# Kernel optimization log

Hardware: AMD Instinct MI355X
Metric: run time of the kernel (lower is better)

## Reference

```python
import jax, jax.numpy as jnp
import numpy as np

B, T, S, A = 8, 256, 16, 1
H, NH, L, NI, TIME, TMAX = 1024, 16, 6, 4096, 8, 512
NEG = -10000.0


def _ln(x, g, b, eps=1e-5):
    m = jnp.mean(x, -1, keepdims=True)
    v = jnp.mean((x - m) ** 2, -1, keepdims=True)
    return (x - m) * jax.lax.rsqrt(v + eps) * g + b


def setup_inputs() -> dict:
    key = jax.random.key(0)
    ks = iter(jax.random.split(key, 64))
    w = lambda *s: 0.02 * jax.random.normal(next(ks), s, jnp.float32)
    inp = {
        'states': jax.random.normal(next(ks), (B, T, S), jnp.float32),
        'actions': jax.random.normal(next(ks), (B, T, A), jnp.float32),
        'rtgs': jax.random.normal(next(ks), (B, T, 1), jnp.float32),
        'attention_mask': jnp.ones((B, T, 1), jnp.float32),
        'state_mean': jnp.zeros((S,), jnp.float32),
        'state_std': jnp.ones((S,), jnp.float32),
        'W_es': w(S, H), 'b_es': jnp.zeros((H,)),
        'W_ea': w(A, H), 'b_ea': jnp.zeros((H,)),
        'W_er': w(1, H), 'b_er': jnp.zeros((H,)),
        'E_t': w(TMAX, TIME),
        'W_ts': w(H + TIME, H), 'b_ts': jnp.zeros((H,)),
        'W_ta': w(H + TIME, H), 'b_ta': jnp.zeros((H,)),
        'W_tr': w(H + TIME, H), 'b_tr': jnp.zeros((H,)),
        'eln_g': jnp.ones((H,)), 'eln_b': jnp.zeros((H,)),
        'ln1_g': jnp.ones((L, H)), 'ln1_b': jnp.zeros((L, H)),
        'ln2_g': jnp.ones((L, H)), 'ln2_b': jnp.zeros((L, H)),
        'Wq': w(L, H, H), 'bq': jnp.zeros((L, H)),
        'Wk': w(L, H, H), 'bk': jnp.zeros((L, H)),
        'Wv': w(L, H, H), 'bv': jnp.zeros((L, H)),
        'Wo': w(L, H, H), 'bo': jnp.zeros((L, H)),
        'W1': w(L, H, NI), 'b1': jnp.zeros((L, NI)),
        'W2': w(L, NI, H), 'b2': jnp.zeros((L, H)),
        'W_pa': w(H, A), 'b_pa': jnp.zeros((A,)),
        'timesteps': jax.random.randint(next(ks), (B, T), 0, TMAX),
    }
    return inp


def _forward(states, actions, rtgs, attention_mask, state_mean, state_std,
             W_es, b_es, W_ea, b_ea, W_er, b_er, E_t,
             W_ts, b_ts, W_ta, b_ta, W_tr, b_tr, eln_g, eln_b,
             ln1_g, ln1_b, ln2_g, ln2_b, Wq, bq, Wk, bk, Wv, bv, Wo, bo,
             W1, b1, W2, b2, W_pa, b_pa, timesteps):
    T3 = 3 * T
    dh = H // NH
    s = (states - state_mean) / (state_std + 1e-9)
    te = E_t[timesteps]                                   # [B,T,8]
    se = jnp.concatenate([s @ W_es + b_es, te], -1) @ W_ts + b_ts
    ae = jnp.concatenate([actions @ W_ea + b_ea, te], -1) @ W_ta + b_ta
    re = jnp.concatenate([rtgs @ W_er + b_er, te], -1) @ W_tr + b_tr
    # interleave (rtg, state, action) per timestep -> [B, 3T, H]
    x = jnp.stack([re, se, ae], axis=2).reshape(B, T3, H)
    x = _ln(x, eln_g, eln_b)

    timestep_mask = jnp.max(attention_mask, axis=-1)      # [B,T]
    pad = (1.0 - jnp.repeat(timestep_mask, 3, axis=1)) * NEG  # [B,3T]
    pad = pad[:, None, None, :]
    causal = jnp.tril(jnp.ones((T3, T3), bool))

    def block(x, p):
        (l1g, l1b, wq, bqv, wk, bkv, wv, bvv, wo, bov,
         l2g, l2b, w1, b1v, w2, b2v) = p
        h = _ln(x, l1g, l1b)
        def heads(w, b):
            return (h @ w + b).reshape(B, T3, NH, dh).transpose(0, 2, 1, 3)
        q, k, v = heads(wq, bqv), heads(wk, bkv), heads(wv, bvv)
        att = jnp.einsum('bhqd,bhkd->bhqk', q, k) / jnp.sqrt(jnp.float32(dh))
        att = jnp.where(causal, att, jnp.asarray(NEG, att.dtype)) + pad
        att = jax.nn.softmax(att, axis=-1)
        y = jnp.einsum('bhqk,bhkd->bhqd', att, v)
        y = y.transpose(0, 2, 1, 3).reshape(B, T3, H) @ wo + bov
        x = x + y
        m = _ln(x, l2g, l2b)
        x = x + jax.nn.gelu(m @ w1 + b1v, approximate=False) @ w2 + b2v
        return x, None

    stacked = (ln1_g, ln1_b, Wq, bq, Wk, bk, Wv, bv, Wo, bo,
               ln2_g, ln2_b, W1, b1, W2, b2)
    x, _ = jax.lax.scan(block, x, stacked)

    x = x.reshape(B, T, 3, H)
    action_preds = x[:, :, 1] @ W_pa + b_pa               # state-token positions
    return action_preds


def reference(states, actions, rtgs, attention_mask, state_mean, state_std,
              W_es, b_es, W_ea, b_ea, W_er, b_er, E_t,
              W_ts, b_ts, W_ta, b_ta, W_tr, b_tr, eln_g, eln_b,
              ln1_g, ln1_b, ln2_g, ln2_b, Wq, bq, Wk, bk, Wv, bv, Wo, bo,
              W1, b1, W2, b2, W_pa, b_pa, timesteps):
    return _forward(states, actions, rtgs, attention_mask, state_mean, state_std,
                    W_es, b_es, W_ea, b_ea, W_er, b_er, E_t,
                    W_ts, b_ts, W_ta, b_ta, W_tr, b_tr, eln_g, eln_b,
                    ln1_g, ln1_b, ln2_g, ln2_b, Wq, bq, Wk, bk, Wv, bv, Wo, bo,
                    W1, b1, W2, b2, W_pa, b_pa, timesteps)
```

## Files before the change

kernel.cpp:

```cpp
#include <hip/hip_runtime.h>
#include <math.h>

#define B_    8
#define T_    256
#define S_    16
#define H_    1024
#define NH_   16
#define L_    6
#define NI_   4096
#define TIME_ 8
#define T3_   768
#define DH_   64
#define BT_   2048
#define ROWS_ 6144
#define KE_   1032
#define KEP_  1056
#define NEGV  (-10000.0f)

typedef unsigned short u16;
typedef short bf16x8 __attribute__((ext_vector_type(8)));
typedef float f32x4 __attribute__((ext_vector_type(4)));

__device__ __forceinline__ float bf2f(u16 u) {
    union { unsigned int i; float f; } x; x.i = ((unsigned int)u) << 16; return x.f;
}
__device__ __forceinline__ u16 f2bf(float f) {
    union { float f; unsigned int i; } x; x.f = f;
    unsigned int r = x.i + 0x7FFFu + ((x.i >> 16) & 1u);
    return (u16)(r >> 16);
}
__device__ __forceinline__ float gelu_fast(float x) {
    float y = 0.7978845608028654f * (x + 0.044715f * x * x * x);
    float e = __expf(2.0f * y);
    float t = 1.0f - 2.0f / (e + 1.0f);
    return 0.5f * x * (1.0f + t);
}

__device__ __forceinline__ void gll16(const u16* g, u16* l) {
    __builtin_amdgcn_global_load_lds(
        (const __attribute__((address_space(1))) unsigned int*)g,
        (__attribute__((address_space(3))) unsigned int*)l,
        16, 0, 0);
}

template <int EPI, int BM>
__device__ __forceinline__ void mgemm_core(
    const u16* __restrict__ A, const u16* __restrict__ Bt,
    const float* __restrict__ bias, float* __restrict__ outf,
    u16* __restrict__ outb, const float* __restrict__ res,
    int N, int K)
{
    constexpr int MT = (BM == 128) ? 4 : 2;
    __shared__ u16 Als[2][BM * 32];
    __shared__ u16 Bls[2][128 * 32];
    const int tid = threadIdx.x;

    const int nbx = N >> 7;
    const int bid = blockIdx.x;
    const int G = nbx << 3;
    const int grp = bid / G;
    const int g = bid - grp * G;
    const int bm = (grp * 8 + (g & 7)) * BM;
    const int bn = (g >> 3) * 128;

    const int lane = tid & 63;
    const int w = tid >> 6;
    const int wr = (BM == 128) ? (w >> 1) : (w & 1);
    const int wc = (BM == 128) ? (w & 1) : (w >> 1);
    const int lrow = lane & 15;
    const int lk = lane >> 4;

    f32x4 acc[MT][4] = {};

    auto stage = [&](int buf, int kk) {
        if (BM == 128) {
            #pragma unroll
            for (int s = 0; s < 2; ++s) {
                const int gb = w * 64 + s * 256;
                const int j = gb >> 7, m0 = gb & 127;
                gll16(A + (size_t)(bm + m0 + lane) * K + kk + j * 8, Als[buf] + gb * 8);
            }
        } else {
            gll16(A + (size_t)(bm + lane) * K + kk + w * 8, Als[buf] + w * 64 * 8);
        }
        #pragma unroll
        for (int s = 0; s < 2; ++s) {
            const int gb = w * 64 + s * 256;
            const int j = gb >> 7, m0 = gb & 127;
            gll16(Bt + (size_t)(bn + m0 + lane) * K + kk + j * 8, Bls[buf] + gb * 8);
        }
    };

    const int niter = K >> 5;
    stage(0, 0);
    for (int i = 0; i < niter; ++i) {
        __syncthreads();
        if (i + 1 < niter) stage((i + 1) & 1, (i + 1) * 32);
        const bf16x8* Af = (const bf16x8*)Als[i & 1];
        const bf16x8* Bf = (const bf16x8*)Bls[i & 1];
        bf16x8 af[MT], bfr[4];
        #pragma unroll
        for (int tm = 0; tm < MT; ++tm)
            af[tm] = Af[lk * BM + wr * (MT * 16) + tm * 16 + lrow];
        #pragma unroll
        for (int tn = 0; tn < 4; ++tn)
            bfr[tn] = Bf[lk * 128 + wc * 64 + tn * 16 + lrow];
        #pragma unroll
        for (int tm = 0; tm < MT; ++tm)
            #pragma unroll
            for (int tn = 0; tn < 4; ++tn)
                acc[tm][tn] = __builtin_amdgcn_mfma_f32_16x16x32_bf16(
                    af[tm], bfr[tn], acc[tm][tn], 0, 0, 0);
    }

    int cg[4]; float bv[4];
    #pragma unroll
    for (int tn = 0; tn < 4; ++tn) {
        cg[tn] = bn + wc * 64 + tn * 16 + lrow;
        bv[tn] = bias[cg[tn]];
    }
    #pragma unroll
    for (int tm = 0; tm < MT; ++tm) {
        const int rbase = bm + wr * (MT * 16) + tm * 16 + lk * 4;
        #pragma unroll
        for (int r = 0; r < 4; ++r) {
            const size_t rowoff = (size_t)(rbase + r) * N;
            #pragma unroll
            for (int tn = 0; tn < 4; ++tn) {
                float v = acc[tm][tn][r] + bv[tn];
                const size_t idx = rowoff + cg[tn];
                if (EPI == 0) outf[idx] = v;
                else if (EPI == 1) outf[idx] = v + res[idx];
                else if (EPI == 2) outb[idx] = f2bf(v);
                else { outb[idx] = f2bf(gelu_fast(v)); }
            }
        }
    }
}

template <int EPI, int BM>
__global__ __launch_bounds__(256) void mgemm(
    const u16* __restrict__ A, const u16* __restrict__ Bt,
    const float* __restrict__ bias, float* __restrict__ outf,
    u16* __restrict__ outb, const float* __restrict__ res,
    int N, int K)
{
    mgemm_core<EPI, BM>(A, Bt, bias, outf, outb, res, N, K);
}

__global__ __launch_bounds__(256) void mgemm_embed(
    const u16* __restrict__ U, const u16* __restrict__ Wt,
    const float* __restrict__ b0, const float* __restrict__ b1,
    const float* __restrict__ b2, float* __restrict__ out)
{
    const int z = blockIdx.z;
    const float* bias = (z == 0) ? b0 : (z == 1) ? b1 : b2;
    mgemm_core<0, 64>(U + (size_t)z * BT_ * KEP_, Wt + (size_t)z * H_ * KEP_,
                      bias, out + (size_t)z * BT_ * H_, nullptr, nullptr,
                      H_, KEP_);
}

__device__ __forceinline__ void convT_core(
    const float* __restrict__ W, u16* __restrict__ Wt, int K, int N, int Kpad)
{
    __shared__ float tile[32][65];
    const int k0 = blockIdx.y * 32, n0 = blockIdx.x * 64;
    const int tid = threadIdx.x;
    #pragma unroll
    for (int p = 0; p < 2; ++p) {
        const int kr = (tid >> 4) + p * 16;
        const int nc = (tid & 15) * 4;
        const int k = k0 + kr;
        float4 v = make_float4(0.f, 0.f, 0.f, 0.f);
        if (k < K) v = *(const float4*)(W + (size_t)k * N + n0 + nc);
        tile[kr][nc + 0] = v.x; tile[kr][nc + 1] = v.y;
        tile[kr][nc + 2] = v.z; tile[kr][nc + 3] = v.w;
    }
    __syncthreads();
    #pragma unroll
    for (int p = 0; p < 2; ++p) {
        const int idx = tid + p * 256;
        const int n = idx >> 3, kq = (idx & 7) * 4;
        ushort4 o;
        o.x = f2bf(tile[kq + 0][n]); o.y = f2bf(tile[kq + 1][n]);
        o.z = f2bf(tile[kq + 2][n]); o.w = f2bf(tile[kq + 3][n]);
        *(ushort4*)(Wt + (size_t)(n0 + n) * Kpad + k0 + kq) = o;
    }
}

__global__ __launch_bounds__(256) void convTv(
    const float* __restrict__ W, u16* __restrict__ Wt, int K, int N, int Kpad)
{
    convT_core(W, Wt, K, N, Kpad);
}

__global__ __launch_bounds__(256) void convT_embed(
    const float* __restrict__ W0, const float* __restrict__ W1,
    const float* __restrict__ W2, u16* __restrict__ Wt)
{
    const int z = blockIdx.z;
    const float* W = (z == 0) ? W0 : (z == 1) ? W1 : W2;
    convT_core(W, Wt + (size_t)z * H_ * KEP_, KE_, H_, KEP_);
}

__global__ __launch_bounds__(256) void convT4v(
    const float* __restrict__ Wq, const float* __restrict__ Wk,
    const float* __restrict__ Wv, const float* __restrict__ Wo,
    const float* __restrict__ bq, const float* __restrict__ bk,
    const float* __restrict__ bv,
    u16* __restrict__ WQKVt, u16* __restrict__ Wot, float* __restrict__ bqkv)
{
    const int z = blockIdx.z;
    const float* W = (z == 0) ? Wq : (z == 1) ? Wk : (z == 2) ? Wv : Wo;
    u16* Wt = (z == 3) ? Wot : WQKVt + (size_t)z * H_ * H_;
    convT_core(W, Wt, H_, H_, H_);
    if (blockIdx.x == 0 && blockIdx.y == 0 && z < 3) {
        const float* bsrc = (z == 0) ? bq : (z == 1) ? bk : bv;
        #pragma unroll
        for (int u = 0; u < 4; ++u) {
            int i = threadIdx.x + u * 256;
            bqkv[z * H_ + i] = bsrc[i];
        }
    }
}

__global__ __launch_bounds__(256) void embed_pre_kernel(
    const float* __restrict__ states, const float* __restrict__ actions,
    const float* __restrict__ rtgs, const float* __restrict__ mean,
    const float* __restrict__ stdv, const float* __restrict__ W_es,
    const float* __restrict__ b_es, const float* __restrict__ W_ea,
    const float* __restrict__ b_ea, const float* __restrict__ W_er,
    const float* __restrict__ b_er, const float* __restrict__ E_t,
    const int* __restrict__ timesteps,
    u16* __restrict__ Us, u16* __restrict__ Ua, u16* __restrict__ Ur)
{
    const int bt  = blockIdx.x;
    const int tid = threadIdx.x;
    __shared__ float sn[S_];
    __shared__ float tev[TIME_];
    if (tid < S_) sn[tid] = (states[bt * S_ + tid] - mean[tid]) / (stdv[tid] + 1e-9f);
    if (tid < TIME_) {
        int ts = timesteps[bt];
        tev[tid] = E_t[ts * TIME_ + tid];
    }
    __syncthreads();
    const float av = actions[bt];
    const float rv = rtgs[bt];
    const size_t rowo = (size_t)bt * KEP_;
    #pragma unroll
    for (int u = 0; u < 4; ++u) {
        int n = tid + u * 256;
        float accs = b_es[n];
        #pragma unroll
        for (int i = 0; i < S_; ++i) accs += sn[i] * W_es[i * H_ + n];
        Us[rowo + n] = f2bf(accs);
        Ua[rowo + n] = f2bf(av * W_ea[n] + b_ea[n]);
        Ur[rowo + n] = f2bf(rv * W_er[n] + b_er[n]);
    }
    if (tid < TIME_) {
        u16 tv = f2bf(tev[tid]);
        Us[rowo + H_ + tid] = tv;
        Ua[rowo + H_ + tid] = tv;
        Ur[rowo + H_ + tid] = tv;
    }
    if (tid < KEP_ - KE_) {
        Us[rowo + KE_ + tid] = 0;
        Ua[rowo + KE_ + tid] = 0;
        Ur[rowo + KE_ + tid] = 0;
    }
}

template <bool BF16OUT>
__device__ __forceinline__ void ln_body(const float* __restrict__ src,
                                        const float* __restrict__ g,
                                        const float* __restrict__ b,
                                        void* __restrict__ dst,
                                        float* red, int tid)
{
    float v[4];
    #pragma unroll
    for (int u = 0; u < 4; ++u) v[u] = src[tid + u * 256];
    float s = v[0] + v[1] + v[2] + v[3];
    red[tid] = s; __syncthreads();
    for (int off = 128; off > 0; off >>= 1) {
        if (tid < off) red[tid] += red[tid + off];
        __syncthreads();
    }
    const float mean = red[0] * (1.0f / H_);
    __syncthreads();
    float ss = 0.0f;
    #pragma unroll
    for (int u = 0; u < 4; ++u) { float d = v[u] - mean; ss += d * d; }
    red[tid] = ss; __syncthreads();
    for (int off = 128; off > 0; off >>= 1) {
        if (tid < off) red[tid] += red[tid + off];
        __syncthreads();
    }
    const float var = red[0] * (1.0f / H_);
    const float rs = rsqrtf(var + 1e-5f);
    #pragma unroll
    for (int u = 0; u < 4; ++u) {
        int col = tid + u * 256;
        float y = (v[u] - mean) * rs * g[col] + b[col];
        if (BF16OUT) ((u16*)dst)[col] = f2bf(y);
        else ((float*)dst)[col] = y;
    }
}

__global__ __launch_bounds__(256) void ln_bf16_kernel(
    const float* __restrict__ X, const float* __restrict__ g,
    const float* __restrict__ b, u16* __restrict__ Y)
{
    __shared__ float red[256];
    const size_t row = blockIdx.x;
    ln_body<true>(X + row * H_, g, b, Y + row * H_, red, threadIdx.x);
}

__global__ __launch_bounds__(256) void interleave_eln_kernel(
    const float* __restrict__ RE, const float* __restrict__ SE,
    const float* __restrict__ AE, const float* __restrict__ g,
    const float* __restrict__ b, float* __restrict__ X)
{
    __shared__ float red[256];
    const int row = blockIdx.x;
    const int bi = row / T3_;
    const int rem = row % T3_;
    const int t = rem / 3, slot = rem % 3;
    const float* src = (slot == 0 ? RE : (slot == 1 ? SE : AE)) + (size_t)(bi * T_ + t) * H_;
    ln_body<false>(src, g, b, X + (size_t)row * H_, red, threadIdx.x);
}

__global__ __launch_bounds__(256) void attn_kernel(
    const u16* __restrict__ QKV, const float* __restrict__ amask,
    u16* __restrict__ Y)
{
    const int qt = blockIdx.x;
    const int h  = blockIdx.y;
    const int b  = blockIdx.z;
    const int tid = threadIdx.x;
    const int lane = tid & 63, w = tid >> 6;
    const int l15 = lane & 15, quad = lane >> 4;

    __shared__ u16 Kls[64][72];
    __shared__ u16 Vt[64][72];
    __shared__ u16 Pls[4][16][72];
    __shared__ float padv[64];

    const u16* Qbase = QKV + (size_t)b * T3_ * 3072 + h * 64;
    const u16* Kbase = Qbase + 1024;
    const u16* Vbase = Qbase + 2048;

    bf16x8 qf[2];
    {
        const u16* qp = Qbase + (size_t)(qt * 64 + w * 16 + l15) * 3072 + quad * 8;
        qf[0] = *(const bf16x8*)qp;
        qf[1] = *(const bf16x8*)(qp + 32);
    }

    float m_i[4], l_i[4];
    f32x4 o[4] = {};
    #pragma unroll
    for (int r = 0; r < 4; ++r) { m_i[r] = -3.0e30f; l_i[r] = 0.0f; }

    const int qr0 = qt * 64 + w * 16 + quad * 4;

    for (int kt = 0; kt <= qt; ++kt) {
        #pragma unroll
        for (int s = 0; s < 2; ++s) {
            const int c = tid + s * 256;
            const int tok = c >> 3, cb = c & 7;
            const size_t go = (size_t)(kt * 64 + tok) * 3072 + cb * 8;
            *(uint4*)&Kls[tok][cb * 8] = *(const uint4*)(Kbase + go);
            uint4 vv = *(const uint4*)(Vbase + go);
            const u16* vs = (const u16*)&vv;
            #pragma unroll
            for (int j = 0; j < 8; ++j) Vt[cb * 8 + j][tok] = vs[j];
        }
        if (tid < 64)
            padv[tid] = (1.0f - amask[b * T_ + (kt * 64 + tid) / 3]) * NEGV;
        __syncthreads();

        f32x4 sacc[4];
        #pragma unroll
        for (int nt = 0; nt < 4; ++nt) {
            bf16x8 kf0 = *(const bf16x8*)&Kls[nt * 16 + l15][quad * 8];
            bf16x8 kf1 = *(const bf16x8*)&Kls[nt * 16 + l15][32 + quad * 8];
            f32x4 z = {};
            z = __builtin_amdgcn_mfma_f32_16x16x32_bf16(qf[0], kf0, z, 0, 0, 0);
            sacc[nt] = __builtin_amdgcn_mfma_f32_16x16x32_bf16(qf[1], kf1, z, 0, 0, 0);
        }

        float sv[4][4];
        float rmax[4] = {-3.0e30f, -3.0e30f, -3.0e30f, -3.0e30f};
        #pragma unroll
        for (int nt = 0; nt < 4; ++nt) {
            const int jc = kt * 64 + nt * 16 + l15;
            const float pv = padv[nt * 16 + l15];
            #pragma unroll
            for (int r = 0; r < 4; ++r) {
                float v = (jc <= qr0 + r) ? sacc[nt][r] * 0.125f : NEGV;
                v += pv;
                sv[nt][r] = v;
                rmax[r] = fmaxf(rmax[r], v);
            }
        }
        #pragma unroll
        for (int m = 1; m < 16; m <<= 1)
            #pragma unroll
            for (int r = 0; r < 4; ++r)
                rmax[r] = fmaxf(rmax[r], __shfl_xor(rmax[r], m, 64));
        float al[4], rsum[4];
        #pragma unroll
        for (int r = 0; r < 4; ++r) {
            const float mn = fmaxf(m_i[r], rmax[r]);
            al[r] = __expf(m_i[r] - mn);
            m_i[r] = mn;
            float sum = 0.0f;
            #pragma unroll
            for (int nt = 0; nt < 4; ++nt) {
                float p = __expf(sv[nt][r] - mn);
                sv[nt][r] = p; sum += p;
            }
            rsum[r] = sum;
        }
        #pragma unroll
        for (int m = 1; m < 16; m <<= 1)
            #pragma unroll
            for (int r = 0; r < 4; ++r)
                rsum[r] += __shfl_xor(rsum[r], m, 64);
        #pragma unroll
        for (int r = 0; r < 4; ++r)
            l_i[r] = l_i[r] * al[r] + rsum[r];

        #pragma unroll
        for (int nt = 0; nt < 4; ++nt)
            #pragma unroll
            for (int r = 0; r < 4; ++r)
                Pls[w][quad * 4 + r][nt * 16 + l15] = f2bf(sv[nt][r]);
        #pragma unroll
        for (int dt = 0; dt < 4; ++dt)
            #pragma unroll
            for (int r = 0; r < 4; ++r)
                o[dt][r] *= al[r];

        bf16x8 pf0 = *(const bf16x8*)&Pls[w][l15][quad * 8];
        bf16x8 pf1 = *(const bf16x8*)&Pls[w][l15][32 + quad * 8];
        #pragma unroll
        for (int dt = 0; dt < 4; ++dt) {
            bf16x8 vf0 = *(const bf16x8*)&Vt[dt * 16 + l15][quad * 8];
            bf16x8 vf1 = *(const bf16x8*)&Vt[dt * 16 + l15][32 + quad * 8];
            o[dt] = __builtin_amdgcn_mfma_f32_16x16x32_bf16(pf0, vf0, o[dt], 0, 0, 0);
            o[dt] = __builtin_amdgcn_mfma_f32_16x16x32_bf16(pf1, vf1, o[dt], 0, 0, 0);
        }
        __syncthreads();
    }

    #pragma unroll
    for (int r = 0; r < 4; ++r) {
        const float inv = 1.0f / l_i[r];
        const size_t row = (size_t)b * T3_ + qt * 64 + w * 16 + quad * 4 + r;
        #pragma unroll
        for (int dt = 0; dt < 4; ++dt)
            Y[row * H_ + h * 64 + dt * 16 + l15] = f2bf(o[dt][r] * inv);
    }
}

__global__ __launch_bounds__(256) void head_kernel(
    const float* __restrict__ X, const float* __restrict__ W_pa,
    const float* __restrict__ b_pa, float* __restrict__ out)
{
    __shared__ float red[256];
    const int row = blockIdx.x;
    const int b = row / T_, t = row % T_;
    const float* x = X + ((size_t)b * T3_ + 3 * t + 1) * H_;
    const int tid = threadIdx.x;
    float s = 0.0f;
    #pragma unroll
    for (int u = 0; u < 4; ++u) {
        int col = tid + u * 256;
        s += x[col] * W_pa[col];
    }
    red[tid] = s; __syncthreads();
    for (int off = 128; off > 0; off >>= 1) {
        if (tid < off) red[tid] += red[tid + off];
        __syncthreads();
    }
    if (tid == 0) out[row] = red[0] + b_pa[0];
}

extern "C" void kernel_launch(void* const* d_in, const int* in_sizes, int n_in,
                              void* d_out, int out_size, void* d_ws, size_t ws_size,
                              hipStream_t stream)
{
    const float* states  = (const float*)d_in[0];
    const float* actions = (const float*)d_in[1];
    const float* rtgs    = (const float*)d_in[2];
    const float* amask   = (const float*)d_in[3];
    const float* smean   = (const float*)d_in[4];
    const float* sstd    = (const float*)d_in[5];
    const float* W_es    = (const float*)d_in[6];
    const float* b_es    = (const float*)d_in[7];
    const float* W_ea    = (const float*)d_in[8];
    const float* b_ea    = (const float*)d_in[9];
    const float* W_er    = (const float*)d_in[10];
    const float* b_er    = (const float*)d_in[11];
    const float* E_t     = (const float*)d_in[12];
    const float* W_ts    = (const float*)d_in[13];
    const float* b_ts    = (const float*)d_in[14];
    const float* W_ta    = (const float*)d_in[15];
    const float* b_ta    = (const float*)d_in[16];
    const float* W_tr    = (const float*)d_in[17];
    const float* b_tr    = (const float*)d_in[18];
    const float* eln_g   = (const float*)d_in[19];
    const float* eln_b   = (const float*)d_in[20];
    const float* ln1_g   = (const float*)d_in[21];
    const float* ln1_b   = (const float*)d_in[22];
    const float* ln2_g   = (const float*)d_in[23];
    const float* ln2_b   = (const float*)d_in[24];
    const float* Wq      = (const float*)d_in[25];
    const float* bq      = (const float*)d_in[26];
    const float* Wk      = (const float*)d_in[27];
    const float* bk      = (const float*)d_in[28];
    const float* Wv      = (const float*)d_in[29];
    const float* bv      = (const float*)d_in[30];
    const float* Wo      = (const float*)d_in[31];
    const float* bo      = (const float*)d_in[32];
    const float* W1      = (const float*)d_in[33];
    const float* b1      = (const float*)d_in[34];
    const float* W2      = (const float*)d_in[35];
    const float* b2      = (const float*)d_in[36];
    const float* W_pa    = (const float*)d_in[37];
    const float* b_pa    = (const float*)d_in[38];
    const int*   tsteps  = (const int*)d_in[39];
    float* out = (float*)d_out;

    char* base = (char*)d_ws;
    float* X    = (float*)base;
    u16*   Hb   = (u16*)(base + 25165824);
    u16*   QKVb = (u16*)(base + 37748736);
    u16*   MIDb = (u16*)(base + 75497472);
    u16*   Wbuf = (u16*)(base + 125829120);

    float* bqkv = (float*)MIDb;
    u16* U_s = MIDb;
    u16* U_a = MIDb + (size_t)BT_ * KEP_;
    u16* U_r = MIDb + (size_t)2 * BT_ * KEP_;
    float* SE = (float*)QKVb;
    float* AE = SE + (size_t)BT_ * H_;
    float* RE = AE + (size_t)BT_ * H_;
    u16* Wemb = Wbuf;

    u16* WQKVt = Wbuf;
    u16* Wot   = Wbuf + (size_t)3072 * 1024;
    u16* W1t   = Wbuf + (size_t)4096 * 1024;
    u16* W2t   = Wbuf + (size_t)8192 * 1024;

    embed_pre_kernel<<<BT_, 256, 0, stream>>>(
        states, actions, rtgs, smean, sstd, W_es, b_es, W_ea, b_ea,
        W_er, b_er, E_t, tsteps, U_s, U_a, U_r);

    dim3 gCvE(H_ / 64, KEP_ / 32, 3);
    convT_embed<<<gCvE, 256, 0, stream>>>(W_ts, W_ta, W_tr, Wemb);

    dim3 gEmb((H_ / 128) * (BT_ / 64), 1, 3);
    mgemm_embed<<<gEmb, 256, 0, stream>>>(U_s, Wemb, b_ts, b_ta, b_tr, SE);

    interleave_eln_kernel<<<ROWS_, 256, 0, stream>>>(RE, SE, AE, eln_g, eln_b, X);

    dim3 gCv4(H_ / 64, H_ / 32, 4);
    dim3 gCvM1(NI_ / 64, H_ / 32);
    dim3 gCvM2(H_ / 64, NI_ / 32);
    const int gQKV = (3072 / 128) * (ROWS_ / 128);
    const int gO   = (H_ / 128) * (ROWS_ / 128);
    const int gM1  = (NI_ / 128) * (ROWS_ / 128);
    dim3 gAttn(T3_ / 64, NH_, B_);

    for (int l = 0; l < L_; ++l) {
        const size_t wOff = (size_t)l * H_ * H_;
        const size_t bOff = (size_t)l * H_;
        const size_t w1Off = (size_t)l * H_ * NI_;
        const size_t b1Off = (size_t)l * NI_;

        convT4v<<<gCv4, 256, 0, stream>>>(
            Wq + wOff, Wk + wOff, Wv + wOff, Wo + wOff,
            bq + bOff, bk + bOff, bv + bOff, WQKVt, Wot, bqkv);
        convTv<<<gCvM1, 256, 0, stream>>>(W1 + w1Off, W1t, H_, NI_, H_);
        convTv<<<gCvM2, 256, 0, stream>>>(W2 + w1Off, W2t, NI_, H_, NI_);

        ln_bf16_kernel<<<ROWS_, 256, 0, stream>>>(X, ln1_g + bOff, ln1_b + bOff, Hb);
        mgemm<2, 128><<<gQKV, 256, 0, stream>>>(Hb, WQKVt, bqkv, nullptr, QKVb, nullptr, 3072, H_);
        attn_kernel<<<gAttn, 256, 0, stream>>>(QKVb, amask, Hb);
        mgemm<1, 128><<<gO, 256, 0, stream>>>(Hb, Wot, bo + bOff, X, nullptr, X, H_, H_);
        ln_bf16_kernel<<<ROWS_, 256, 0, stream>>>(X, ln2_g + bOff, ln2_b + bOff, Hb);
        mgemm<3, 128><<<gM1, 256, 0, stream>>>(Hb, W1t, b1 + b1Off, nullptr, MIDb, nullptr, NI_, H_);
        mgemm<1, 128><<<gO, 256, 0, stream>>>(MIDb, W2t, b2 + bOff, X, nullptr, X, H_, NI_);
    }

    head_kernel<<<BT_, 256, 0, stream>>>(X, W_pa, b_pa, out);
}
```

Baseline: 3.206 ms.

## Split-K the Wo and W2 GEMMs with atomic accumulation into residual

Adds a split-K variant of the bf16 MFMA GEMM that divides K across two blockIdx.y slices and accumulates partial tiles directly into the fp32 residual stream with atomic adds. Only split 0 adds the bias. It is used for the output-projection and second MLP GEMMs, which have N=1024 and only 384 tiles, so the grid doubles to fill the CUs better. The cost is atomic traffic to X and non-deterministic summation order.

```diff
diff --git a/kernel.cpp b/kernel.cpp
--- a/kernel.cpp
+++ b/kernel.cpp
@@ -48,7 +48,7 @@
     const u16* __restrict__ A, const u16* __restrict__ Bt,
     const float* __restrict__ bias, float* __restrict__ outf,
     u16* __restrict__ outb, const float* __restrict__ res,
-    int N, int K)
+    int N, int K, int koff, int klen, bool addb)
 {
     constexpr int MT = (BM == 128) ? 4 : 2;
     __shared__ u16 Als[2][BM * 32];
@@ -91,11 +91,11 @@
         }
     };
 
-    const int niter = K >> 5;
-    stage(0, 0);
+    const int niter = klen >> 5;
+    stage(0, koff);
     for (int i = 0; i < niter; ++i) {
         __syncthreads();
-        if (i + 1 < niter) stage((i + 1) & 1, (i + 1) * 32);
+        if (i + 1 < niter) stage((i + 1) & 1, koff + (i + 1) * 32);
         const bf16x8* Af = (const bf16x8*)Als[i & 1];
         const bf16x8* Bf = (const bf16x8*)Bls[i & 1];
         bf16x8 af[MT], bfr[4];
@@ -117,7 +117,7 @@
     #pragma unroll
     for (int tn = 0; tn < 4; ++tn) {
         cg[tn] = bn + wc * 64 + tn * 16 + lrow;
-        bv[tn] = bias[cg[tn]];
+        bv[tn] = addb ? bias[cg[tn]] : 0.0f;
     }
     #pragma unroll
     for (int tm = 0; tm < MT; ++tm) {
@@ -132,7 +132,8 @@
                 if (EPI == 0) outf[idx] = v;
                 else if (EPI == 1) outf[idx] = v + res[idx];
                 else if (EPI == 2) outb[idx] = f2bf(v);
-                else { outb[idx] = f2bf(gelu_fast(v)); }
+                else if (EPI == 3) { outb[idx] = f2bf(gelu_fast(v)); }
+                else { unsafeAtomicAdd(outf + idx, v); }
             }
         }
     }
@@ -145,7 +146,20 @@
     u16* __restrict__ outb, const float* __restrict__ res,
     int N, int K)
 {
-    mgemm_core<EPI, BM>(A, Bt, bias, outf, outb, res, N, K);
+    mgemm_core<EPI, BM>(A, Bt, bias, outf, outb, res, N, K, 0, K, true);
+}
+
+template <int EPI, int BM>
+__global__ __launch_bounds__(256) void mgemm_sk(
+    const u16* __restrict__ A, const u16* __restrict__ Bt,
+    const float* __restrict__ bias, float* __restrict__ outf,
+    u16* __restrict__ outb, const float* __restrict__ res,
+    int N, int K, int nsplit)
+{
+    const int split = blockIdx.y;
+    const int klen = K / nsplit;
+    mgemm_core<EPI, BM>(A, Bt, bias, outf, outb, res, N, K,
+                        split * klen, klen, split == 0);
 }
 
 __global__ __launch_bounds__(256) void mgemm_embed(
@@ -157,7 +171,7 @@
     const float* bias = (z == 0) ? b0 : (z == 1) ? b1 : b2;
     mgemm_core<0, 64>(U + (size_t)z * BT_ * KEP_, Wt + (size_t)z * H_ * KEP_,
                       bias, out + (size_t)z * BT_ * H_, nullptr, nullptr,
-                      H_, KEP_);
+                      H_, KEP_, 0, KEP_, true);
 }
 
 __device__ __forceinline__ void convT_core(
@@ -571,8 +585,8 @@
     dim3 gCvM1(NI_ / 64, H_ / 32);
     dim3 gCvM2(H_ / 64, NI_ / 32);
     const int gQKV = (3072 / 128) * (ROWS_ / 128);
-    const int gO   = (H_ / 128) * (ROWS_ / 128);
     const int gM1  = (NI_ / 128) * (ROWS_ / 128);
+    dim3 gOsk((H_ / 128) * (ROWS_ / 128), 2);
     dim3 gAttn(T3_ / 64, NH_, B_);
 
     for (int l = 0; l < L_; ++l) {
@@ -590,10 +604,10 @@
         ln_bf16_kernel<<<ROWS_, 256, 0, stream>>>(X, ln1_g + bOff, ln1_b + bOff, Hb);
         mgemm<2, 128><<<gQKV, 256, 0, stream>>>(Hb, WQKVt, bqkv, nullptr, QKVb, nullptr, 3072, H_);
         attn_kernel<<<gAttn, 256, 0, stream>>>(QKVb, amask, Hb);
-        mgemm<1, 128><<<gO, 256, 0, stream>>>(Hb, Wot, bo + bOff, X, nullptr, X, H_, H_);
+        mgemm_sk<4, 128><<<gOsk, 256, 0, stream>>>(Hb, Wot, bo + bOff, X, nullptr, nullptr, H_, H_, 2);
         ln_bf16_kernel<<<ROWS_, 256, 0, stream>>>(X, ln2_g + bOff, ln2_b + bOff, Hb);
         mgemm<3, 128><<<gM1, 256, 0, stream>>>(Hb, W1t, b1 + b1Off, nullptr, MIDb, nullptr, NI_, H_);
-        mgemm<1, 128><<<gO, 256, 0, stream>>>(MIDb, W2t, b2 + bOff, X, nullptr, X, H_, NI_);
+        mgemm_sk<4, 128><<<gOsk, 256, 0, stream>>>(MIDb, W2t, b2 + bOff, X, nullptr, nullptr, H_, NI_, 2);
     }
 
     head_kernel<<<BT_, 256, 0, stream>>>(X, W_pa, b_pa, out);
```

Result: slower. 3.302 ms (+3.0%).
